# Kernel tuning notes

Hardware: AMD Instinct MI355X
Metric: run time of the kernel (lower is better)

## Reference

```python
import jax, jax.numpy as jnp
import numpy as np

DIM = 512
NUM_HEAD = 8
HEAD_DIM = DIM // NUM_HEAD
FFN = 4 * DIM


def setup_inputs() -> dict:
    key = jax.random.key(0)
    ks = jax.random.split(key, 16)
    s = DIM ** -0.5
    inp = {
        "x": jax.random.normal(ks[0], (4, 2048, DIM), jnp.float32),
        "wq": jax.random.normal(ks[1], (DIM, DIM), jnp.float32) * s,
        "bq": jnp.zeros((DIM,), jnp.float32),
        "wk": jax.random.normal(ks[2], (DIM, DIM), jnp.float32) * s,
        "bk": jnp.zeros((DIM,), jnp.float32),
        "wv": jax.random.normal(ks[3], (DIM, DIM), jnp.float32) * s,
        "bv": jnp.zeros((DIM,), jnp.float32),
        "wo": jax.random.normal(ks[4], (DIM, DIM), jnp.float32) * s,
        "bo": jnp.zeros((DIM,), jnp.float32),
        "w1": jax.random.normal(ks[5], (DIM, FFN), jnp.float32) * s,
        "b1": jnp.zeros((FFN,), jnp.float32),
        "w2": jax.random.normal(ks[6], (FFN, DIM), jnp.float32) * (FFN ** -0.5),
        "b2": jnp.zeros((DIM,), jnp.float32),
        "g1": jnp.ones((DIM,), jnp.float32),
        "be1": jnp.zeros((DIM,), jnp.float32),
        "g2": jnp.ones((DIM,), jnp.float32),
        "be2": jnp.zeros((DIM,), jnp.float32),
    }
    return inp


def layer_norm(x, g, b, eps=1e-5):
    mu = jnp.mean(x, axis=-1, keepdims=True)
    var = jnp.var(x, axis=-1, keepdims=True)
    return (x - mu) * jax.lax.rsqrt(var + eps) * g + b


def _forward(x, wq, bq, wk, bk, wv, bv, wo, bo, w1, b1, w2, b2, g1, be1, g2, be2):
    b, n, _ = x.shape
    scale = HEAD_DIM ** -0.5
    q = (x @ wq + bq).reshape(b, n, NUM_HEAD, HEAD_DIM).transpose(0, 2, 1, 3)
    k = (x @ wk + bk).reshape(b, n, NUM_HEAD, HEAD_DIM).transpose(0, 2, 1, 3)
    v = (x @ wv + bv).reshape(b, n, NUM_HEAD, HEAD_DIM).transpose(0, 2, 1, 3)
    scores = jnp.einsum('bhqd,bhkd->bhqk', q, k) * scale
    attn = jax.nn.softmax(scores, axis=-1)
    out = jnp.einsum('bhqk,bhkd->bhqd', attn, v)
    out = out.transpose(0, 2, 1, 3).reshape(b, n, DIM)
    out = out @ wo + bo
    x = layer_norm(out + x, g1, be1)
    h = jax.nn.gelu(x @ w1 + b1, approximate=False)
    ff = h @ w2 + b2
    x = layer_norm(ff + x, g2, be2)
    return x


def reference(x, wq, bq, wk, bk, wv, bv, wo, bo, w1, b1, w2, b2, g1, be1, g2, be2):
    return _forward(x, wq, bq, wk, bk, wv, bv, wo, bo, w1, b1, w2, b2, g1, be1, g2, be2)
```

## Files before the change

### kernel.cpp

```cpp
#include <hip/hip_runtime.h>
#include <math.h>

#define DIM 512
#define NHEAD 8
#define HD 64
#define FFN_DIM 2048
#define BATCH 4
#define SEQ 2048
#define MTOK (BATCH*SEQ)

typedef __attribute__((ext_vector_type(8))) short bf16x8;
typedef __attribute__((ext_vector_type(4))) short bf16x4;
typedef __attribute__((ext_vector_type(4))) float f32x4;

__device__ __forceinline__ unsigned short f2b(float f){
    unsigned int u = __float_as_uint(f);
    u += 0x7fffu + ((u >> 16) & 1u);
    return (unsigned short)(u >> 16);
}
__device__ __forceinline__ float b2f(unsigned short u){
    return __uint_as_float(((unsigned int)u) << 16);
}
__device__ __forceinline__ unsigned int pack_trunc(float f0, float f1){
    return __builtin_amdgcn_perm(__float_as_uint(f1), __float_as_uint(f0), 0x07060302u);
}
__device__ __forceinline__ void async_cp16(const unsigned short* g, unsigned short* l){
    __builtin_amdgcn_global_load_lds((const __attribute__((address_space(1))) unsigned int*)g,
                                     (__attribute__((address_space(3))) unsigned int*)l, 16, 0, 0);
}
__device__ __forceinline__ f32x4 mfma16(bf16x4 a, bf16x4 b, f32x4 c){
    asm("v_mfma_f32_16x16x16_bf16 %0, %1, %2, %0" : "+v"(c) : "v"(a), "v"(b));
    return c;
}
__device__ __forceinline__ float gelu_fast(float x){
    float x3 = x*x*x;
    float y  = 2.302588f * (x + 0.044715f*x3);
    float t  = __builtin_amdgcn_exp2f(y);
    return x * t * __builtin_amdgcn_rcpf(t + 1.0f);
}

__device__ __forceinline__ void transp32(const float* __restrict__ in, unsigned short* __restrict__ out,
                                         int N, int K, int n0_rd, int n0_wr, int k0,
                                         unsigned short (&t)[32][33], int tid){
    int tx = tid & 31, ty = tid >> 5;
    #pragma unroll
    for (int u = 0; u < 4; u++)
        t[tx][ty + 8*u] = f2b(in[(size_t)(k0 + ty + 8*u)*N + n0_rd + tx]);
    __syncthreads();
    #pragma unroll
    for (int u = 0; u < 4; u++)
        out[(size_t)(n0_wr + ty + 8*u)*K + k0 + tx] = t[ty + 8*u][tx];
}

__global__ void prep_kernel(const float* __restrict__ x,
                            const float* __restrict__ wq, const float* __restrict__ wk,
                            const float* __restrict__ wv, const float* __restrict__ wo,
                            const float* __restrict__ w1, const float* __restrict__ w2,
                            const float* __restrict__ bq, const float* __restrict__ bk,
                            const float* __restrict__ bv,
                            unsigned short* __restrict__ xb, unsigned short* __restrict__ wqkvT,
                            unsigned short* __restrict__ woT, unsigned short* __restrict__ w1T,
                            unsigned short* __restrict__ w2T, float* __restrict__ bqkv)
{
    __shared__ unsigned short t[32][33];
    int bid = blockIdx.x, tid = threadIdx.x;
    if (bid < 4096) {
        int i = (bid*256 + tid)*4;
        float4 v = *(const float4*)(x + i);
        ushort4 o; o.x=f2b(v.x); o.y=f2b(v.y); o.z=f2b(v.z); o.w=f2b(v.w);
        *(ushort4*)(xb + i) = o;
    } else if (bid < 4864) {
        int r = bid - 4096;
        int n0 = (r % 48)*32, k0 = (r / 48)*32;
        const float* w = (n0 < 512) ? wq : (n0 < 1024) ? wk : wv;
        transp32(w, wqkvT, 512, 512, n0 & 511, n0, k0, t, tid);
    } else if (bid < 5120) {
        int r = bid - 4864;
        int n0 = (r % 16)*32, k0 = (r / 16)*32;
        transp32(wo, woT, 512, 512, n0, n0, k0, t, tid);
    } else if (bid < 6144) {
        int r = bid - 5120;
        int n0 = (r % 64)*32, k0 = (r / 64)*32;
        transp32(w1, w1T, 2048, 512, n0, n0, k0, t, tid);
    } else if (bid < 7168) {
        int r = bid - 6144;
        int n0 = (r % 16)*32, k0 = (r / 16)*32;
        transp32(w2, w2T, 512, 2048, n0, n0, k0, t, tid);
    } else {
        int i = (bid - 7168)*256 + tid;
        if (i < 1536)
            bqkv[i] = (i < 512) ? bq[i] : (i < 1024) ? bk[i-512] : bv[i-1024];
    }
}

template<int MODE, int SK>
__global__ __launch_bounds__(256, 4)
void gemm_bf16(const unsigned short* __restrict__ A, const unsigned short* __restrict__ Bt,
               const float* __restrict__ bias,
               unsigned short* __restrict__ Cb,
               unsigned short* __restrict__ qo, unsigned short* __restrict__ ko,
               unsigned short* __restrict__ vTo,
               int M, int N, int K)
{
    __shared__ unsigned short As[128*64];
    __shared__ unsigned short Bs[128*64];
    int tid  = threadIdx.x;
    int lane = tid & 63;
    int ln = lane & 15, qd = lane >> 4;
    int m0 = blockIdx.x * 128, n0 = blockIdx.y * 128;
    int wid = tid >> 6;
    int wm = (wid >> 1) * 64;
    int wn = (wid & 1) * 64;
    int kbeg = (SK > 1) ? (int)blockIdx.z * (K/SK) : 0;
    int kend = kbeg + K/SK;
    if (SK > 1 && MODE == 0) Cb += (size_t)blockIdx.z * M * N;

    f32x4 acc[4][4];
    #pragma unroll
    for (int i = 0; i < 4; i++)
        #pragma unroll
        for (int j = 0; j < 4; j++) acc[i][j] = (f32x4){0.f,0.f,0.f,0.f};

    for (int k0 = kbeg; k0 < kend; k0 += 64) {
        #pragma unroll
        for (int i = 0; i < 4; i++) {
            int cid = i*256 + tid;
            int row = cid >> 3, cs = cid & 7;
            int cg = cs ^ (row & 7);
            async_cp16(&A[(size_t)(m0+row)*K + k0 + cg*8], &As[(cid & ~63) * 8]);
        }
        #pragma unroll
        for (int i = 0; i < 4; i++) {
            int cid = i*256 + tid;
            int row = cid >> 3, cs = cid & 7;
            int cg = cs ^ (row & 7);
            async_cp16(&Bt[(size_t)(n0+row)*K + k0 + cg*8], &Bs[(cid & ~63) * 8]);
        }
        __syncthreads();
        #pragma unroll
        for (int kk = 0; kk < 64; kk += 32) {
            int c0 = kk >> 3;
            bf16x8 af[4], bf[4];
            #pragma unroll
            for (int t = 0; t < 4; t++)
                af[t] = *(bf16x8*)&As[(wm + t*16 + ln)*64 + ((c0 + qd) ^ (ln & 7))*8];
            #pragma unroll
            for (int t = 0; t < 4; t++)
                bf[t] = *(bf16x8*)&Bs[(wn + t*16 + ln)*64 + ((c0 + qd) ^ (ln & 7))*8];
            #pragma unroll
            for (int i = 0; i < 4; i++)
                #pragma unroll
                for (int j = 0; j < 4; j++)
                    acc[i][j] = __builtin_amdgcn_mfma_f32_16x16x32_bf16(af[i], bf[j], acc[i][j], 0,0,0);
        }
        __syncthreads();
    }

    const float QSCALE = 0.18033688011112042f;
    #pragma unroll
    for (int i = 0; i < 4; i++) {
        int mb = m0 + wm + i*16 + qd*4;
        #pragma unroll
        for (int j = 0; j < 4; j++) {
            int c = n0 + wn + j*16 + ln;
            float bv_ = (SK > 1 && blockIdx.z) ? 0.f : bias[c];
            float v[4];
            #pragma unroll
            for (int r = 0; r < 4; r++) v[r] = acc[i][j][r] + bv_;
            if (MODE == 0) {
                #pragma unroll
                for (int r = 0; r < 4; r++) Cb[(size_t)(mb+r)*N + c] = f2b(v[r]);
            } else if (MODE == 2) {
                #pragma unroll
                for (int r = 0; r < 4; r++)
                    Cb[(size_t)(mb+r)*N + c] = f2b(gelu_fast(v[r]));
            } else {
                int b = mb >> 11, t0 = mb & 2047;
                if (c < 512) {
                    int h = c >> 6, hd = c & 63;
                    #pragma unroll
                    for (int r = 0; r < 4; r++)
                        qo[(((size_t)(b*8 + h))*SEQ + t0 + r)*64 + hd] = f2b(v[r] * QSCALE);
                } else if (c < 1024) {
                    int cc = c - 512, h = cc >> 6, hd = cc & 63;
                    #pragma unroll
                    for (int r = 0; r < 4; r++)
                        ko[(((size_t)(b*8 + h))*SEQ + t0 + r)*64 + hd] = f2b(v[r]);
                } else {
                    int cc = c - 1024, h = cc >> 6, hd = cc & 63;
                    ushort4 pk;
                    pk.x = f2b(v[0]); pk.y = f2b(v[1]); pk.z = f2b(v[2]); pk.w = f2b(v[3]);
                    *(ushort4*)&vTo[(((size_t)(b*8 + h))*64 + hd)*SEQ + t0] = pk;
                }
            }
        }
    }
}

__global__ __launch_bounds__(256)
void attn_mfma(const unsigned short* __restrict__ Q, const unsigned short* __restrict__ K,
               const unsigned short* __restrict__ VT, unsigned short* __restrict__ O)
{
    __shared__ unsigned short lds[24576];
    int tid  = threadIdx.x;
    int wid  = tid >> 6, lane = tid & 63;
    int ln = lane & 15, qd = lane >> 4;
    int bx = blockIdx.x;
    int qb = (bx >> 3) & 15;
    int bh = (bx & 7) + 8 * (bx >> 7);

    #pragma unroll
    for (int i = 0; i < 4; i++) {
        int cid = i*256 + tid;
        int row = cid >> 3, cs = cid & 7, cg = cs ^ (row & 7);
        async_cp16(&Q[((size_t)bh*SEQ + qb*128 + row)*64 + cg*8], &lds[16384 + (cid & ~63)*8]);
    }
    #pragma unroll
    for (int t = 0; t < 2; t++) {
        #pragma unroll
        for (int i = 0; i < 2; i++) {
            int cid = i*256 + tid;
            int row = cid >> 3, cs = cid & 7, cg = cs ^ (row & 7);
            async_cp16(&K [((size_t)bh*SEQ + t*64 + row)*64 + cg*8], &lds[t*8192 + (cid & ~63)*8]);
            async_cp16(&VT[((size_t)bh*64 + row)*SEQ + t*64 + cg*8], &lds[t*8192 + 4096 + (cid & ~63)*8]);
        }
    }
    asm volatile("s_waitcnt vmcnt(8)" ::: "memory");
    __builtin_amdgcn_s_barrier();
    __builtin_amdgcn_sched_barrier(0);

    bf16x8 qf[2][2];
    #pragma unroll
    for (int qs = 0; qs < 2; qs++)
        #pragma unroll
        for (int kk = 0; kk < 2; kk++)
            qf[qs][kk] = *(bf16x8*)&lds[16384 + (wid*32 + qs*16 + ln)*64 + ((kk*4 + qd) ^ (ln & 7))*8];
    asm volatile("s_waitcnt lgkmcnt(0)" ::: "memory");
    __builtin_amdgcn_sched_barrier(0);

    f32x4 o[2][4];
    #pragma unroll
    for (int qs = 0; qs < 2; qs++)
        #pragma unroll
        for (int dt = 0; dt < 4; dt++) o[qs][dt] = (f32x4){0.f,0.f,0.f,0.f};
    float l_i[2] = {0.f, 0.f};

    for (int kt = 0; kt < 32; kt++) {
        if (kt < 31) { asm volatile("s_waitcnt vmcnt(4)" ::: "memory"); }
        else         { asm volatile("s_waitcnt vmcnt(0)" ::: "memory"); }
        __builtin_amdgcn_s_barrier();
        __builtin_amdgcn_sched_barrier(0);
        if (kt < 30) {
            int nb = ((kt+2) % 3) * 8192;
            #pragma unroll
            for (int i = 0; i < 2; i++) {
                int cid = i*256 + tid;
                int row = cid >> 3, cs = cid & 7, cg = cs ^ (row & 7);
                async_cp16(&K [((size_t)bh*SEQ + (kt+2)*64 + row)*64 + cg*8], &lds[nb + (cid & ~63)*8]);
                async_cp16(&VT[((size_t)bh*64 + row)*SEQ + (kt+2)*64 + cg*8], &lds[nb + 4096 + (cid & ~63)*8]);
            }
        }
        int kof = (kt % 3) * 8192;
        int vof = kof + 4096;

        f32x4 s[2][4];
        #pragma unroll
        for (int qs = 0; qs < 2; qs++)
            #pragma unroll
            for (int nt = 0; nt < 4; nt++) s[qs][nt] = (f32x4){0.f,0.f,0.f,0.f};
        #pragma unroll
        for (int kk = 0; kk < 2; kk++) {
            #pragma unroll
            for (int nt = 0; nt < 4; nt++) {
                bf16x8 kf = *(bf16x8*)&lds[kof + (nt*16 + ln)*64 + ((kk*4 + qd) ^ (ln & 7))*8];
                s[0][nt] = __builtin_amdgcn_mfma_f32_16x16x32_bf16(kf, qf[0][kk], s[0][nt], 0,0,0);
                s[1][nt] = __builtin_amdgcn_mfma_f32_16x16x32_bf16(kf, qf[1][kk], s[1][nt], 0,0,0);
            }
        }

        bf16x4 pf[2][4];
        #pragma unroll
        for (int qs = 0; qs < 2; qs++) {
            #pragma unroll
            for (int nt = 0; nt < 4; nt++) {
                float p0 = __builtin_amdgcn_exp2f(s[qs][nt][0]);
                float p1 = __builtin_amdgcn_exp2f(s[qs][nt][1]);
                float p2 = __builtin_amdgcn_exp2f(s[qs][nt][2]);
                float p3 = __builtin_amdgcn_exp2f(s[qs][nt][3]);
                l_i[qs] += (p0 + p1) + (p2 + p3);
                uint2 pk;
                pk.x = pack_trunc(p0, p1);
                pk.y = pack_trunc(p2, p3);
                pf[qs][nt] = __builtin_bit_cast(bf16x4, pk);
            }
        }

        #pragma unroll
        for (int nt = 0; nt < 4; nt++) {
            #pragma unroll
            for (int dt = 0; dt < 4; dt++) {
                bf16x4 vf = *(bf16x4*)&lds[vof + (dt*16 + ln)*64
                                           + ((nt*2 + (qd>>1)) ^ (ln & 7))*8 + (qd & 1)*4];
                o[0][dt] = mfma16(vf, pf[0][nt], o[0][dt]);
                o[1][dt] = mfma16(vf, pf[1][nt], o[1][dt]);
            }
        }
    }
    asm volatile("s_nop 7");
    asm volatile("s_nop 7");

    int b = bh >> 3, h = bh & 7;
    #pragma unroll
    for (int qs = 0; qs < 2; qs++) {
        float l = l_i[qs];
        l += __shfl_xor(l, 16);
        l += __shfl_xor(l, 32);
        float linv = 1.0f / l;
        int t = qb*128 + wid*32 + qs*16 + ln;
        #pragma unroll
        for (int dt = 0; dt < 4; dt++) {
            ushort4 pk;
            pk.x = f2b(o[qs][dt][0]*linv); pk.y = f2b(o[qs][dt][1]*linv);
            pk.z = f2b(o[qs][dt][2]*linv); pk.w = f2b(o[qs][dt][3]*linv);
            *(ushort4*)&O[((size_t)b*SEQ + t)*DIM + h*64 + dt*16 + qd*4] = pk;
        }
    }
}

__global__ void ln1_kernel(const unsigned short* __restrict__ m0b, const unsigned short* __restrict__ m1b,
                           const float* __restrict__ resp,
                           const float* __restrict__ g, const float* __restrict__ be,
                           unsigned short* __restrict__ outb)
{
    int row  = blockIdx.x*4 + (threadIdx.x >> 6);
    int lane = threadIdx.x & 63;
    size_t base = (size_t)row * DIM + lane*8;

    ushort4 a0 = *(const ushort4*)(m0b + base);
    ushort4 a1 = *(const ushort4*)(m0b + base + 4);
    ushort4 c0 = *(const ushort4*)(m1b + base);
    ushort4 c1 = *(const ushort4*)(m1b + base + 4);
    float4 r0 = *(const float4*)(resp + base);
    float4 r1 = *(const float4*)(resp + base + 4);
    float v[8] = { b2f(a0.x)+b2f(c0.x)+r0.x, b2f(a0.y)+b2f(c0.y)+r0.y,
                   b2f(a0.z)+b2f(c0.z)+r0.z, b2f(a0.w)+b2f(c0.w)+r0.w,
                   b2f(a1.x)+b2f(c1.x)+r1.x, b2f(a1.y)+b2f(c1.y)+r1.y,
                   b2f(a1.z)+b2f(c1.z)+r1.z, b2f(a1.w)+b2f(c1.w)+r1.w };
    float s = 0.f, s2 = 0.f;
    #pragma unroll
    for (int i = 0; i < 8; i++) { s += v[i]; s2 += v[i]*v[i]; }
    #pragma unroll
    for (int d = 32; d >= 1; d >>= 1) { s += __shfl_xor(s, d); s2 += __shfl_xor(s2, d); }
    float mean = s * (1.0f / DIM);
    float rstd = rsqrtf(s2 * (1.0f / DIM) - mean*mean + 1e-5f);

    float4 g0 = *(const float4*)(g + lane*8);
    float4 g1 = *(const float4*)(g + lane*8 + 4);
    float4 b0 = *(const float4*)(be + lane*8);
    float4 b1 = *(const float4*)(be + lane*8 + 4);
    float gg[8] = {g0.x,g0.y,g0.z,g0.w,g1.x,g1.y,g1.z,g1.w};
    float bb[8] = {b0.x,b0.y,b0.z,b0.w,b1.x,b1.y,b1.z,b1.w};
    float o[8];
    #pragma unroll
    for (int i = 0; i < 8; i++) o[i] = (v[i]-mean)*rstd*gg[i] + bb[i];
    ushort4 p0, p1;
    p0.x=f2b(o[0]); p0.y=f2b(o[1]); p0.z=f2b(o[2]); p0.w=f2b(o[3]);
    p1.x=f2b(o[4]); p1.y=f2b(o[5]); p1.z=f2b(o[6]); p1.w=f2b(o[7]);
    *(ushort4*)(outb + base)     = p0;
    *(ushort4*)(outb + base + 4) = p1;
}

__global__ void ln2_kernel(const unsigned short* __restrict__ m0b, const unsigned short* __restrict__ m1b,
                           const unsigned short* __restrict__ resb,
                           const float* __restrict__ g, const float* __restrict__ be,
                           float* __restrict__ outf)
{
    int row  = blockIdx.x*4 + (threadIdx.x >> 6);
    int lane = threadIdx.x & 63;
    size_t base = (size_t)row * DIM + lane*8;

    ushort4 a0 = *(const ushort4*)(m0b + base);
    ushort4 a1 = *(const ushort4*)(m0b + base + 4);
    ushort4 c0 = *(const ushort4*)(m1b + base);
    ushort4 c1 = *(const ushort4*)(m1b + base + 4);
    ushort4 rb0 = *(const ushort4*)(resb + base);
    ushort4 rb1 = *(const ushort4*)(resb + base + 4);
    float v[8] = { b2f(a0.x)+b2f(c0.x)+b2f(rb0.x), b2f(a0.y)+b2f(c0.y)+b2f(rb0.y),
                   b2f(a0.z)+b2f(c0.z)+b2f(rb0.z), b2f(a0.w)+b2f(c0.w)+b2f(rb0.w),
                   b2f(a1.x)+b2f(c1.x)+b2f(rb1.x), b2f(a1.y)+b2f(c1.y)+b2f(rb1.y),
                   b2f(a1.z)+b2f(c1.z)+b2f(rb1.z), b2f(a1.w)+b2f(c1.w)+b2f(rb1.w) };
    float s = 0.f, s2 = 0.f;
    #pragma unroll
    for (int i = 0; i < 8; i++) { s += v[i]; s2 += v[i]*v[i]; }
    #pragma unroll
    for (int d = 32; d >= 1; d >>= 1) { s += __shfl_xor(s, d); s2 += __shfl_xor(s2, d); }
    float mean = s * (1.0f / DIM);
    float rstd = rsqrtf(s2 * (1.0f / DIM) - mean*mean + 1e-5f);

    float4 g0 = *(const float4*)(g + lane*8);
    float4 g1 = *(const float4*)(g + lane*8 + 4);
    float4 b0 = *(const float4*)(be + lane*8);
    float4 b1 = *(const float4*)(be + lane*8 + 4);
    float gg[8] = {g0.x,g0.y,g0.z,g0.w,g1.x,g1.y,g1.z,g1.w};
    float bb[8] = {b0.x,b0.y,b0.z,b0.w,b1.x,b1.y,b1.z,b1.w};
    float o[8];
    #pragma unroll
    for (int i = 0; i < 8; i++) o[i] = (v[i] - mean)*rstd*gg[i] + bb[i];
    *(float4*)(outf + base)     = (float4){o[0],o[1],o[2],o[3]};
    *(float4*)(outf + base + 4) = (float4){o[4],o[5],o[6],o[7]};
}

extern "C" void kernel_launch(void* const* d_in, const int* in_sizes, int n_in,
                              void* d_out, int out_size, void* d_ws, size_t ws_size,
                              hipStream_t stream) {
    const float* x   = (const float*)d_in[0];
    const float* wq  = (const float*)d_in[1];
    const float* bq  = (const float*)d_in[2];
    const float* wk  = (const float*)d_in[3];
    const float* bk  = (const float*)d_in[4];
    const float* wv  = (const float*)d_in[5];
    const float* bv  = (const float*)d_in[6];
    const float* wo  = (const float*)d_in[7];
    const float* bo  = (const float*)d_in[8];
    const float* w1  = (const float*)d_in[9];
    const float* b1  = (const float*)d_in[10];
    const float* w2  = (const float*)d_in[11];
    const float* b2  = (const float*)d_in[12];
    const float* g1  = (const float*)d_in[13];
    const float* be1 = (const float*)d_in[14];
    const float* g2  = (const float*)d_in[15];
    const float* be2 = (const float*)d_in[16];
    float* out = (float*)d_out;

    char* w = (char*)d_ws;
    size_t off = 0;
    auto alloc = [&](size_t bytes){ void* p = w + off; off += (bytes + 255) & ~(size_t)255; return p; };
    unsigned short* xb     = (unsigned short*)alloc((size_t)MTOK*DIM*2);
    unsigned short* wqkvT  = (unsigned short*)alloc((size_t)1536*512*2);
    unsigned short* woT    = (unsigned short*)alloc((size_t)512*512*2);
    unsigned short* w1T    = (unsigned short*)alloc((size_t)2048*512*2);
    unsigned short* w2T    = (unsigned short*)alloc((size_t)512*2048*2);
    float*          bqkv   = (float*)alloc(1536*4);
    unsigned short* qb_    = (unsigned short*)alloc((size_t)32*SEQ*64*2);
    unsigned short* kb_    = (unsigned short*)alloc((size_t)32*SEQ*64*2);
    unsigned short* vT_    = (unsigned short*)alloc((size_t)32*64*SEQ*2);
    unsigned short* attno  = (unsigned short*)alloc((size_t)MTOK*DIM*2);
    unsigned short* x1b    = (unsigned short*)alloc((size_t)MTOK*DIM*2);
    unsigned short* h_     = (unsigned short*)alloc((size_t)MTOK*FFN_DIM*2);
    unsigned short* ffb    = (unsigned short*)alloc((size_t)2*MTOK*DIM*2);

    prep_kernel<<<7174, 256, 0, stream>>>(x, wq, wk, wv, wo, w1, w2, bq, bk, bv,
                                          xb, wqkvT, woT, w1T, w2T, bqkv);

    gemm_bf16<1,1><<<dim3(64,12), 256, 0, stream>>>(xb, wqkvT, bqkv, nullptr,
                                                    qb_, kb_, vT_, MTOK, 1536, DIM);
    attn_mfma<<<512, 256, 0, stream>>>(qb_, kb_, vT_, attno);
    gemm_bf16<0,2><<<dim3(64,4,2), 256, 0, stream>>>(attno, woT, bo, ffb,
                                                     nullptr, nullptr, nullptr, MTOK, DIM, DIM);
    ln1_kernel<<<MTOK/4, 256, 0, stream>>>(ffb, ffb + (size_t)MTOK*DIM, x, g1, be1, x1b);
    gemm_bf16<2,1><<<dim3(64,16), 256, 0, stream>>>(x1b, w1T, b1, h_,
                                                    nullptr, nullptr, nullptr, MTOK, FFN_DIM, DIM);
    gemm_bf16<0,2><<<dim3(64,4,2), 256, 0, stream>>>(h_, w2T, b2, ffb,
                                                     nullptr, nullptr, nullptr, MTOK, DIM, FFN_DIM);
    ln2_kernel<<<MTOK/4, 256, 0, stream>>>(ffb, ffb + (size_t)MTOK*DIM, x1b, g2, be2, out);
}
```

Before: 252.8 us.

## Split attention key tiles across two wave groups with 512-thread blocks

Doubles the attention block to 512 threads. Each half of the waves processes half of every 64-key tile for the same 128 queries, and the partial outputs and row sums are merged through LDS at the end. Q fragments are now loaded directly from global memory into registers instead of being staged through LDS, and s_setprio is raised around the MFMA sections. The aim is more waves per CU to hide latency and less per-wave work per tile, at the cost of an extra LDS reduction and barrier at the end and launch bounds that may limit registers.

Result: faster. 240.8 us (-4.8%).

```diff
diff --git a/kernel.cpp b/kernel.cpp
--- a/kernel.cpp
+++ b/kernel.cpp
@@ -197,7 +197,7 @@
     }
 }
 
-__global__ __launch_bounds__(256)
+__global__ __launch_bounds__(512, 4)
 void attn_mfma(const unsigned short* __restrict__ Q, const unsigned short* __restrict__ K,
                const unsigned short* __restrict__ VT, unsigned short* __restrict__ O)
 {
@@ -205,38 +205,26 @@
     int tid  = threadIdx.x;
     int wid  = tid >> 6, lane = tid & 63;
     int ln = lane & 15, qd = lane >> 4;
+    int wq = wid & 3;
+    int wk = wid >> 2;
     int bx = blockIdx.x;
     int qb = (bx >> 3) & 15;
     int bh = (bx & 7) + 8 * (bx >> 7);
 
-    #pragma unroll
-    for (int i = 0; i < 4; i++) {
-        int cid = i*256 + tid;
-        int row = cid >> 3, cs = cid & 7, cg = cs ^ (row & 7);
-        async_cp16(&Q[((size_t)bh*SEQ + qb*128 + row)*64 + cg*8], &lds[16384 + (cid & ~63)*8]);
-    }
+    bf16x8 qf[2][2];
+    #pragma unroll
+    for (int qs = 0; qs < 2; qs++)
+        #pragma unroll
+        for (int kk = 0; kk < 2; kk++)
+            qf[qs][kk] = *(const bf16x8*)&Q[((size_t)bh*SEQ + qb*128 + wq*32 + qs*16 + ln)*64 + kk*32 + qd*8];
+
+    int srow = tid >> 3, scs = tid & 7, scg = scs ^ (srow & 7);
+    int sdst = (tid & ~63) * 8;
     #pragma unroll
     for (int t = 0; t < 2; t++) {
-        #pragma unroll
-        for (int i = 0; i < 2; i++) {
-            int cid = i*256 + tid;
-            int row = cid >> 3, cs = cid & 7, cg = cs ^ (row & 7);
-            async_cp16(&K [((size_t)bh*SEQ + t*64 + row)*64 + cg*8], &lds[t*8192 + (cid & ~63)*8]);
-            async_cp16(&VT[((size_t)bh*64 + row)*SEQ + t*64 + cg*8], &lds[t*8192 + 4096 + (cid & ~63)*8]);
-        }
-    }
-    asm volatile("s_waitcnt vmcnt(8)" ::: "memory");
-    __builtin_amdgcn_s_barrier();
-    __builtin_amdgcn_sched_barrier(0);
-
-    bf16x8 qf[2][2];
-    #pragma unroll
-    for (int qs = 0; qs < 2; qs++)
-        #pragma unroll
-        for (int kk = 0; kk < 2; kk++)
-            qf[qs][kk] = *(bf16x8*)&lds[16384 + (wid*32 + qs*16 + ln)*64 + ((kk*4 + qd) ^ (ln & 7))*8];
-    asm volatile("s_waitcnt lgkmcnt(0)" ::: "memory");
-    __builtin_amdgcn_sched_barrier(0);
+        async_cp16(&K [((size_t)bh*SEQ + t*64 + srow)*64 + scg*8], &lds[t*8192 + sdst]);
+        async_cp16(&VT[((size_t)bh*64 + srow)*SEQ + t*64 + scg*8], &lds[t*8192 + 4096 + sdst]);
+    }
 
     f32x4 o[2][4];
     #pragma unroll
@@ -246,83 +234,111 @@
     float l_i[2] = {0.f, 0.f};
 
     for (int kt = 0; kt < 32; kt++) {
-        if (kt < 31) { asm volatile("s_waitcnt vmcnt(4)" ::: "memory"); }
+        if (kt < 31) { asm volatile("s_waitcnt vmcnt(2)" ::: "memory"); }
         else         { asm volatile("s_waitcnt vmcnt(0)" ::: "memory"); }
         __builtin_amdgcn_s_barrier();
         __builtin_amdgcn_sched_barrier(0);
         if (kt < 30) {
             int nb = ((kt+2) % 3) * 8192;
-            #pragma unroll
-            for (int i = 0; i < 2; i++) {
-                int cid = i*256 + tid;
-                int row = cid >> 3, cs = cid & 7, cg = cs ^ (row & 7);
-                async_cp16(&K [((size_t)bh*SEQ + (kt+2)*64 + row)*64 + cg*8], &lds[nb + (cid & ~63)*8]);
-                async_cp16(&VT[((size_t)bh*64 + row)*SEQ + (kt+2)*64 + cg*8], &lds[nb + 4096 + (cid & ~63)*8]);
-            }
+            async_cp16(&K [((size_t)bh*SEQ + (kt+2)*64 + srow)*64 + scg*8], &lds[nb + sdst]);
+            async_cp16(&VT[((size_t)bh*64 + srow)*SEQ + (kt+2)*64 + scg*8], &lds[nb + 4096 + sdst]);
         }
         int kof = (kt % 3) * 8192;
         int vof = kof + 4096;
 
-        f32x4 s[2][4];
+        bf16x8 kf[2][2];
+        #pragma unroll
+        for (int ntl = 0; ntl < 2; ntl++)
+            #pragma unroll
+            for (int kk = 0; kk < 2; kk++)
+                kf[ntl][kk] = *(bf16x8*)&lds[kof + (wk*32 + ntl*16 + ln)*64 + ((kk*4 + qd) ^ (ln & 7))*8];
+        f32x4 s[2][2];
         #pragma unroll
         for (int qs = 0; qs < 2; qs++)
             #pragma unroll
-            for (int nt = 0; nt < 4; nt++) s[qs][nt] = (f32x4){0.f,0.f,0.f,0.f};
+            for (int ntl = 0; ntl < 2; ntl++) s[qs][ntl] = (f32x4){0.f,0.f,0.f,0.f};
+        __builtin_amdgcn_s_setprio(1);
         #pragma unroll
         for (int kk = 0; kk < 2; kk++) {
             #pragma unroll
-            for (int nt = 0; nt < 4; nt++) {
-                bf16x8 kf = *(bf16x8*)&lds[kof + (nt*16 + ln)*64 + ((kk*4 + qd) ^ (ln & 7))*8];
-                s[0][nt] = __builtin_amdgcn_mfma_f32_16x16x32_bf16(kf, qf[0][kk], s[0][nt], 0,0,0);
-                s[1][nt] = __builtin_amdgcn_mfma_f32_16x16x32_bf16(kf, qf[1][kk], s[1][nt], 0,0,0);
+            for (int ntl = 0; ntl < 2; ntl++) {
+                s[0][ntl] = __builtin_amdgcn_mfma_f32_16x16x32_bf16(kf[ntl][kk], qf[0][kk], s[0][ntl], 0,0,0);
+                s[1][ntl] = __builtin_amdgcn_mfma_f32_16x16x32_bf16(kf[ntl][kk], qf[1][kk], s[1][ntl], 0,0,0);
             }
         }
-
-        bf16x4 pf[2][4];
+        __builtin_amdgcn_s_setprio(0);
+
+        bf16x4 pf[2][2];
         #pragma unroll
         for (int qs = 0; qs < 2; qs++) {
             #pragma unroll
-            for (int nt = 0; nt < 4; nt++) {
-                float p0 = __builtin_amdgcn_exp2f(s[qs][nt][0]);
-                float p1 = __builtin_amdgcn_exp2f(s[qs][nt][1]);
-                float p2 = __builtin_amdgcn_exp2f(s[qs][nt][2]);
-                float p3 = __builtin_amdgcn_exp2f(s[qs][nt][3]);
+            for (int ntl = 0; ntl < 2; ntl++) {
+                float p0 = __builtin_amdgcn_exp2f(s[qs][ntl][0]);
+                float p1 = __builtin_amdgcn_exp2f(s[qs][ntl][1]);
+                float p2 = __builtin_amdgcn_exp2f(s[qs][ntl][2]);
+                float p3 = __builtin_amdgcn_exp2f(s[qs][ntl][3]);
                 l_i[qs] += (p0 + p1) + (p2 + p3);
                 uint2 pk;
                 pk.x = pack_trunc(p0, p1);
                 pk.y = pack_trunc(p2, p3);
-                pf[qs][nt] = __builtin_bit_cast(bf16x4, pk);
+                pf[qs][ntl] = __builtin_bit_cast(bf16x4, pk);
             }
         }
 
-        #pragma unroll
-        for (int nt = 0; nt < 4; nt++) {
+        __builtin_amdgcn_s_setprio(1);
+        #pragma unroll
+        for (int ntl = 0; ntl < 2; ntl++) {
             #pragma unroll
             for (int dt = 0; dt < 4; dt++) {
                 bf16x4 vf = *(bf16x4*)&lds[vof + (dt*16 + ln)*64
-                                           + ((nt*2 + (qd>>1)) ^ (ln & 7))*8 + (qd & 1)*4];
-                o[0][dt] = mfma16(vf, pf[0][nt], o[0][dt]);
-                o[1][dt] = mfma16(vf, pf[1][nt], o[1][dt]);
+                                           + ((wk*4 + ntl*2 + (qd>>1)) ^ (ln & 7))*8 + (qd & 1)*4];
+                o[0][dt] = mfma16(vf, pf[0][ntl], o[0][dt]);
+                o[1][dt] = mfma16(vf, pf[1][ntl], o[1][dt]);
             }
         }
+        __builtin_amdgcn_s_setprio(0);
     }
     asm volatile("s_nop 7");
     asm volatile("s_nop 7");
 
-    int b = bh >> 3, h = bh & 7;
+    float l[2];
     #pragma unroll
     for (int qs = 0; qs < 2; qs++) {
-        float l = l_i[qs];
-        l += __shfl_xor(l, 16);
-        l += __shfl_xor(l, 32);
-        float linv = 1.0f / l;
-        int t = qb*128 + wid*32 + qs*16 + ln;
-        #pragma unroll
-        for (int dt = 0; dt < 4; dt++) {
-            ushort4 pk;
-            pk.x = f2b(o[qs][dt][0]*linv); pk.y = f2b(o[qs][dt][1]*linv);
-            pk.z = f2b(o[qs][dt][2]*linv); pk.w = f2b(o[qs][dt][3]*linv);
-            *(ushort4*)&O[((size_t)b*SEQ + t)*DIM + h*64 + dt*16 + qd*4] = pk;
+        float t = l_i[qs];
+        t += __shfl_xor(t, 16);
+        t += __shfl_xor(t, 32);
+        l[qs] = t;
+    }
+
+    __syncthreads();
+    float* fl = (float*)lds;
+    if (wk == 1) {
+        #pragma unroll
+        for (int qs = 0; qs < 2; qs++) {
+            #pragma unroll
+            for (int dt = 0; dt < 4; dt++)
+                *(f32x4*)&fl[(((wq*2 + qs)*4 + dt)*64 + lane)*4] = o[qs][dt];
+            fl[8192 + (wq*2 + qs)*64 + lane] = l[qs];
+        }
+    }
+    __syncthreads();
+    if (wk == 0) {
+        int b = bh >> 3, h = bh & 7;
+        #pragma unroll
+        for (int qs = 0; qs < 2; qs++) {
+            float lt = l[qs] + fl[8192 + (wq*2 + qs)*64 + lane];
+            float linv = 1.0f / lt;
+            int t = qb*128 + wq*32 + qs*16 + ln;
+            #pragma unroll
+            for (int dt = 0; dt < 4; dt++) {
+                f32x4 po = *(f32x4*)&fl[(((wq*2 + qs)*4 + dt)*64 + lane)*4];
+                ushort4 pk;
+                pk.x = f2b((o[qs][dt][0] + po[0])*linv);
+                pk.y = f2b((o[qs][dt][1] + po[1])*linv);
+                pk.z = f2b((o[qs][dt][2] + po[2])*linv);
+                pk.w = f2b((o[qs][dt][3] + po[3])*linv);
+                *(ushort4*)&O[((size_t)b*SEQ + t)*DIM + h*64 + dt*16 + qd*4] = pk;
+            }
         }
     }
 }
@@ -454,7 +470,7 @@
 
     gemm_bf16<1,1><<<dim3(64,12), 256, 0, stream>>>(xb, wqkvT, bqkv, nullptr,
                                                     qb_, kb_, vT_, MTOK, 1536, DIM);
-    attn_mfma<<<512, 256, 0, stream>>>(qb_, kb_, vT_, attno);
+    attn_mfma<<<512, 512, 0, stream>>>(qb_, kb_, vT_, attno);
     gemm_bf16<0,2><<<dim3(64,4,2), 256, 0, stream>>>(attno, woT, bo, ffb,
                                                      nullptr, nullptr, nullptr, MTOK, DIM, DIM);
     ln1_kernel<<<MTOK/4, 256, 0, stream>>>(ffb, ffb + (size_t)MTOK*DIM, x, g1, be1, x1b);
```
